# Kernel optimization log

Measured on AMD Instinct MI355X. Metric: run time of the kernel, lower is better.

The kernel has to match this reference:

```python
import jax, jax.numpy as jnp
import numpy as np

N, E, H, R = 50000, 800000, 256, 8
LN_EPS = 1e-5


def setup_inputs() -> dict:
    key = jax.random.key(0)
    ks = jax.random.split(key, 6)
    node_states = jax.random.normal(ks[0], (N, H), dtype=jnp.float32)
    edge_index = jax.random.randint(ks[1], (2, E), 0, N, dtype=jnp.int64)
    edge_type_ids = jax.random.randint(ks[2], (E,), 0, R, dtype=jnp.int64)
    scale = 1.0 / np.sqrt(H)
    W_rel = jax.random.normal(ks[3], (R, H, H), dtype=jnp.float32) * scale
    W_root = jax.random.normal(ks[4], (H, H), dtype=jnp.float32) * scale
    bias = jnp.zeros((H,), dtype=jnp.float32)
    ln_gamma = jnp.ones((H,), dtype=jnp.float32)
    ln_beta = jnp.zeros((H,), dtype=jnp.float32)
    return {
        "node_states": node_states,
        "edge_index": edge_index,
        "edge_type_ids": edge_type_ids,
        "W_rel": W_rel,
        "W_root": W_root,
        "bias": bias,
        "ln_gamma": ln_gamma,
        "ln_beta": ln_beta,
    }


def _rgcn_layer(node_states, edge_index, edge_type_ids, W_rel, W_root, bias, ln_gamma, ln_beta):
    n, h = node_states.shape
    r = W_rel.shape[0]
    src, dst = edge_index[0], edge_index[1]
    # Per-(dst, relation) MEAN of source features (PyG RGCNConv default aggr='mean').
    seg = dst * r + edge_type_ids  # composite segment id in [0, N*R)
    msgs = node_states[src]  # [E, H] gather
    sums = jax.ops.segment_sum(msgs, seg, num_segments=n * r).reshape(n, r, h)
    counts = jax.ops.segment_sum(jnp.ones((src.shape[0],), node_states.dtype), seg,
                                 num_segments=n * r).reshape(n, r, 1)
    mean = sums / jnp.maximum(counts, 1.0)  # zero-edge buckets stay 0
    # Relation-specific linear transforms applied to aggregated means, then root + bias.
    agg = jnp.einsum('nrh,rho->no', mean, W_rel)
    conv = agg + node_states @ W_root + bias
    # Exact (erf-based) GELU to match torch.nn.functional.gelu default.
    updated = jax.nn.gelu(conv, approximate=False)
    # Dropout is identity in eval mode.
    x = updated + node_states  # residual
    mu = jnp.mean(x, axis=-1, keepdims=True)
    var = jnp.mean(jnp.square(x - mu), axis=-1, keepdims=True)
    return ln_gamma * (x - mu) * jax.lax.rsqrt(var + LN_EPS) + ln_beta


def reference(node_states, edge_index, edge_type_ids, W_rel, W_root, bias, ln_gamma, ln_beta):
    return _rgcn_layer(node_states, edge_index, edge_type_ids, W_rel, W_root, bias, ln_gamma, ln_beta)
```

## Files before the change

### kernel.cpp

```cpp
#include <hip/hip_runtime.h>
#include <cstdint>
#include <cstddef>

#define N_NODES 50000
#define N_EDGES 800000
#define HDIM    256
#define NREL    8
#define NSEG    (N_NODES * NREL)
#define KDIM    (NREL * HDIM + HDIM)
#define KA      (NREL * HDIM)
#define LN_EPSF 1e-5f

#define SCAN_CHUNK 1024
#define SCAN_NB    ((NSEG + SCAN_CHUNK - 1) / SCAN_CHUNK)

using short8  = __attribute__((ext_vector_type(8))) short;
using ushort8 = __attribute__((ext_vector_type(8))) unsigned short;
using float4v = __attribute__((ext_vector_type(4))) float;

static __device__ __forceinline__ unsigned short f2bf(float f) {
    union { float f; uint32_t i; } v; v.f = f;
    uint32_t r = v.i + 0x7FFFu + ((v.i >> 16) & 1u);
    return (unsigned short)(r >> 16);
}
static __device__ __forceinline__ float bf2f(unsigned short u) {
    union { uint32_t i; float f; } v; v.i = ((uint32_t)u) << 16; return v.f;
}

__global__ __launch_bounds__(256) void k_cast(const float* __restrict__ ns,
                                              unsigned short* __restrict__ ns16) {
    int idx = blockIdx.x * blockDim.x + threadIdx.x;
    if (idx >= N_NODES * HDIM / 8) return;
    const float4v* nsv = (const float4v*)ns;
    float4v v0 = nsv[idx * 2], v1 = nsv[idx * 2 + 1];
    ushort8 o;
    o[0] = f2bf(v0[0]); o[1] = f2bf(v0[1]); o[2] = f2bf(v0[2]); o[3] = f2bf(v0[3]);
    o[4] = f2bf(v1[0]); o[5] = f2bf(v1[1]); o[6] = f2bf(v1[2]); o[7] = f2bf(v1[3]);
    *(ushort8*)&ns16[(size_t)idx * 8] = o;
}

__global__ void k_count(const int* __restrict__ ei, const int* __restrict__ et,
                        int* __restrict__ cnt) {
    int e = blockIdx.x * blockDim.x + threadIdx.x;
    if (e >= N_EDGES) return;
    int dst = ei[N_EDGES + e];
    int rel = et[e];
    atomicAdd(&cnt[dst * NREL + rel], 1);
}

__global__ __launch_bounds__(256) void k_scan1(const int* __restrict__ cnt,
                                               int* __restrict__ bsum) {
    int b = blockIdx.x, t = threadIdx.x;
    int idx = b * SCAN_CHUNK + t * 4;
    int4 v = {0, 0, 0, 0};
    if (idx + 3 < NSEG) v = *(const int4*)&cnt[idx];
    else {
        #pragma unroll
        for (int j = 0; j < 4; ++j) if (idx + j < NSEG) ((int*)&v)[j] = cnt[idx + j];
    }
    int s = v.x + v.y + v.z + v.w;
    #pragma unroll
    for (int o = 32; o > 0; o >>= 1) s += __shfl_xor(s, o, 64);
    __shared__ int ls[4];
    if ((t & 63) == 0) ls[t >> 6] = s;
    __syncthreads();
    if (t == 0) bsum[b] = ls[0] + ls[1] + ls[2] + ls[3];
}

__global__ __launch_bounds__(512) void k_scan2(const int* __restrict__ bsum,
                                               int* __restrict__ boff) {
    __shared__ int s[512];
    int t = threadIdx.x;
    int v = (t < SCAN_NB) ? bsum[t] : 0;
    s[t] = v;
    __syncthreads();
    for (int d = 1; d < 512; d <<= 1) {
        int x = (t >= d) ? s[t - d] : 0;
        __syncthreads();
        s[t] += x;
        __syncthreads();
    }
    if (t < SCAN_NB) boff[t] = s[t] - v;
}

__global__ __launch_bounds__(256) void k_scan3(const int* __restrict__ cnt,
                                               const int* __restrict__ boff,
                                               int* __restrict__ off) {
    int b = blockIdx.x, t = threadIdx.x;
    int idx = b * SCAN_CHUNK + t * 4;
    int4 v = {0, 0, 0, 0};
    if (idx + 3 < NSEG) v = *(const int4*)&cnt[idx];
    else {
        #pragma unroll
        for (int j = 0; j < 4; ++j) if (idx + j < NSEG) ((int*)&v)[j] = cnt[idx + j];
    }
    int s = v.x + v.y + v.z + v.w;
    __shared__ int ls[256];
    ls[t] = s;
    __syncthreads();
    for (int d = 1; d < 256; d <<= 1) {
        int x = (t >= d) ? ls[t - d] : 0;
        __syncthreads();
        ls[t] += x;
        __syncthreads();
    }
    int run = boff[b] + ls[t] - s;
    int4 w;
    w.x = run; run += v.x;
    w.y = run; run += v.y;
    w.z = run; run += v.z;
    w.w = run;
    if (idx + 3 < NSEG) *(int4*)&off[idx] = w;
    else {
        #pragma unroll
        for (int j = 0; j < 4; ++j) if (idx + j < NSEG) off[idx + j] = ((int*)&w)[j];
    }
    if (b == 0 && t == 0) off[NSEG] = N_EDGES;
}

__global__ void k_scatter(const int* __restrict__ ei, const int* __restrict__ et,
                          const int* __restrict__ off, int* __restrict__ cursor,
                          int* __restrict__ srcs) {
    int e = blockIdx.x * blockDim.x + threadIdx.x;
    if (e >= N_EDGES) return;
    int src = ei[e];
    int dst = ei[N_EDGES + e];
    int rel = et[e];
    int seg = dst * NREL + rel;
    int pos = off[seg] + atomicAdd(&cursor[seg], 1);
    srcs[pos] = src;
}

__global__ __launch_bounds__(256) void k_aggregate(const unsigned short* __restrict__ ns16,
                                                   const int* __restrict__ off,
                                                   const int* __restrict__ srcs,
                                                   unsigned short* __restrict__ Afull) {
    int n = blockIdx.x, t = threadIdx.x;
    int g = t >> 5;
    int i = t & 31;
    int seg = n * NREL + g;
    int e0 = off[seg], e1 = off[seg + 1];
    int cnt = e1 - e0;
    int cs = cnt < 32 ? cnt : 32;
    int my_src = (i < cs) ? srcs[e0 + i] : 0;

    const ushort8* nsv = (const ushort8*)ns16;
    float acc[8] = {0.f, 0.f, 0.f, 0.f, 0.f, 0.f, 0.f, 0.f};

    for (int k = 0; k < cs; ++k) {
        int src = __shfl(my_src, k, 32);
        ushort8 v = nsv[(size_t)src * 32 + i];
        #pragma unroll
        for (int j = 0; j < 8; ++j) acc[j] += bf2f(v[j]);
    }
    for (int e = e0 + 32; e < e1; ++e) {
        int src = srcs[e];
        ushort8 v = nsv[(size_t)src * 32 + i];
        #pragma unroll
        for (int j = 0; j < 8; ++j) acc[j] += bf2f(v[j]);
    }

    float inv = (cnt > 0) ? 1.0f / (float)cnt : 0.0f;
    ushort8 wv;
    #pragma unroll
    for (int j = 0; j < 8; ++j) wv[j] = f2bf(acc[j] * inv);
    *(ushort8*)&Afull[(size_t)n * KDIM + g * HDIM + i * 8] = wv;
}

__global__ __launch_bounds__(256) void k_buildB(const float* __restrict__ Wrel,
                                                const float* __restrict__ Wroot,
                                                unsigned short* __restrict__ Bt) {
    __shared__ unsigned short tile[64][66];
    int k0 = blockIdx.x * 64;
    int j0 = blockIdx.y * 64;
    int t = threadIdx.x;

    #pragma unroll
    for (int p = 0; p < 16; ++p) {
        int idx = p * 256 + t;
        int kk = idx >> 6, jj = idx & 63;
        int k = k0 + kk;
        float v;
        if (k < NREL * HDIM) {
            int r = k >> 8, h = k & 255;
            v = Wrel[((size_t)r * HDIM + h) * HDIM + (j0 + jj)];
        } else {
            int h = k - NREL * HDIM;
            v = Wroot[(size_t)h * HDIM + (j0 + jj)];
        }
        tile[kk][jj] = f2bf(v);
    }
    __syncthreads();
    #pragma unroll
    for (int p = 0; p < 16; ++p) {
        int idx = p * 256 + t;
        int jj = idx >> 6, kk = idx & 63;
        Bt[(size_t)(j0 + jj) * KDIM + (k0 + kk)] = tile[kk][jj];
    }
}

#define BM 128
#define BN 256
#define BK 64
#define NITER (KDIM / BK)

__global__ __launch_bounds__(512, 4) void k_gemm(const unsigned short* __restrict__ A,
                                                 const unsigned short* __restrict__ ns16,
                                                 const unsigned short* __restrict__ Bt,
                                                 const float* __restrict__ ns,
                                                 const float* __restrict__ bias,
                                                 const float* __restrict__ gamma,
                                                 const float* __restrict__ beta,
                                                 float* __restrict__ out, int M) {
    __shared__ __align__(16) unsigned short As[BM * BK];
    __shared__ __align__(16) unsigned short Bs[BN * BK];
    __shared__ float s1buf[BM][4], s2buf[BM][4];

    int tid  = threadIdx.x;
    int lane = tid & 63;
    int wid  = tid >> 6;
    int wm   = wid >> 2, wn = wid & 3;
    int brow = blockIdx.x * BM;

    float4v acc[4][4] = {};

    const char* Ab = (const char*)A;
    const char* Nb = (const char*)ns16;
    const char* Bb = (const char*)Bt;
    const size_t rstride = (size_t)KDIM * 2;

    for (int kt = 0; kt < KDIM; kt += BK) {
        #pragma unroll
        for (int i = 0; i < 2; ++i) {
            int linear = i * 8192 + tid * 16;
            int row  = linear >> 7;
            int slot = (linear >> 4) & 7;
            int kb   = (slot ^ (row & 7)) * 16;
            int ra = brow + row; if (ra > M - 1) ra = M - 1;
            const char* ga = (kt < KA)
                ? Ab + (size_t)ra * rstride + (size_t)(kt * 2 + kb)
                : Nb + (size_t)ra * (HDIM * 2) + (size_t)((kt - KA) * 2 + kb);
            __builtin_amdgcn_global_load_lds(
                (const __attribute__((address_space(1))) void*)ga,
                (__attribute__((address_space(3))) void*)((char*)As + linear),
                16, 0, 0);
        }
        #pragma unroll
        for (int i = 0; i < 4; ++i) {
            int linear = i * 8192 + tid * 16;
            int row  = linear >> 7;
            int slot = (linear >> 4) & 7;
            int kb   = (slot ^ (row & 7)) * 16;
            const char* gb = Bb + (size_t)row * rstride + (size_t)(kt * 2 + kb);
            __builtin_amdgcn_global_load_lds(
                (const __attribute__((address_space(1))) void*)gb,
                (__attribute__((address_space(3))) void*)((char*)Bs + linear),
                16, 0, 0);
        }
        __syncthreads();

        #pragma unroll
        for (int h = 0; h < 2; ++h) {
            short8 a[4], b[4];
            int s0 = h * 4 + (lane >> 4);
            #pragma unroll
            for (int m = 0; m < 4; ++m) {
                int r = wm * 64 + m * 16 + (lane & 15);
                a[m] = *(const short8*)((const char*)As + r * 128 + ((s0 ^ (r & 7)) * 16));
            }
            #pragma unroll
            for (int n = 0; n < 4; ++n) {
                int r = wn * 64 + n * 16 + (lane & 15);
                b[n] = *(const short8*)((const char*)Bs + r * 128 + ((s0 ^ (r & 7)) * 16));
            }
            #pragma unroll
            for (int m = 0; m < 4; ++m)
                #pragma unroll
                for (int n = 0; n < 4; ++n)
                    acc[m][n] = __builtin_amdgcn_mfma_f32_16x16x32_bf16(a[m], b[n], acc[m][n], 0, 0, 0);
        }
        __syncthreads();
    }

    int cols[4];
    float bias_v[4];
    #pragma unroll
    for (int n = 0; n < 4; ++n) {
        cols[n] = wn * 64 + n * 16 + (lane & 15);
        bias_v[n] = bias[cols[n]];
    }

    #pragma unroll
    for (int m = 0; m < 4; ++m) {
        #pragma unroll
        for (int q = 0; q < 4; ++q) {
            int lr = wm * 64 + m * 16 + (lane >> 4) * 4 + q;
            int r  = brow + lr;
            float s1 = 0.f, s2 = 0.f;
            #pragma unroll
            for (int n = 0; n < 4; ++n) {
                float conv = acc[m][n][q] + bias_v[n];
                float g = 0.5f * conv * (1.0f + erff(conv * 0.70710678118654752f));
                float resid = (r < M) ? ns[(size_t)r * HDIM + cols[n]] : 0.f;
                float x = g + resid;
                acc[m][n][q] = x;
                s1 += x; s2 += x * x;
            }
            #pragma unroll
            for (int o = 8; o > 0; o >>= 1) {
                s1 += __shfl_xor(s1, o, 64);
                s2 += __shfl_xor(s2, o, 64);
            }
            if ((lane & 15) == 0) { s1buf[lr][wn] = s1; s2buf[lr][wn] = s2; }
        }
    }
    __syncthreads();

    float gam[4], bet[4];
    #pragma unroll
    for (int n = 0; n < 4; ++n) { gam[n] = gamma[cols[n]]; bet[n] = beta[cols[n]]; }

    #pragma unroll
    for (int m = 0; m < 4; ++m) {
        #pragma unroll
        for (int q = 0; q < 4; ++q) {
            int lr = wm * 64 + m * 16 + (lane >> 4) * 4 + q;
            int r  = brow + lr;
            float t1 = s1buf[lr][0] + s1buf[lr][1] + s1buf[lr][2] + s1buf[lr][3];
            float t2 = s2buf[lr][0] + s2buf[lr][1] + s2buf[lr][2] + s2buf[lr][3];
            float mu  = t1 * (1.0f / HDIM);
            float var = t2 * (1.0f / HDIM) - mu * mu;
            float rstd = rsqrtf(var + LN_EPSF);
            if (r < M) {
                #pragma unroll
                for (int n = 0; n < 4; ++n) {
                    float x = acc[m][n][q];
                    out[(size_t)r * HDIM + cols[n]] = gam[n] * (x - mu) * rstd + bet[n];
                }
            }
        }
    }
}

extern "C" void kernel_launch(void* const* d_in, const int* in_sizes, int n_in,
                              void* d_out, int out_size, void* d_ws, size_t ws_size,
                              hipStream_t stream) {
    const float* ns    = (const float*)d_in[0];
    const int*   ei    = (const int*)d_in[1];
    const int*   et    = (const int*)d_in[2];
    const float* Wrel  = (const float*)d_in[3];
    const float* Wroot = (const float*)d_in[4];
    const float* bias  = (const float*)d_in[5];
    const float* gamma = (const float*)d_in[6];
    const float* beta  = (const float*)d_in[7];
    float* out = (float*)d_out;

    char* w = (char*)d_ws;
    auto take = [&](size_t bytes) -> char* {
        char* p = w; w += (bytes + 255) & ~(size_t)255; return p;
    };
    int* cnt              = (int*)take((size_t)NSEG * 4);
    int* segoff           = (int*)take((size_t)(NSEG + 1) * 4);
    int* cursor           = (int*)take((size_t)NSEG * 4);
    int* srcs             = (int*)take((size_t)N_EDGES * 4);
    int* bsum             = (int*)take((size_t)SCAN_NB * 4);
    int* boff             = (int*)take((size_t)SCAN_NB * 4);
    unsigned short* Afull = (unsigned short*)take((size_t)N_NODES * KDIM * 2);
    unsigned short* Bt    = (unsigned short*)take((size_t)HDIM * KDIM * 2);
    unsigned short* ns16  = (unsigned short*)take((size_t)N_NODES * HDIM * 2);

    hipMemsetAsync(cnt, 0, (size_t)NSEG * 4, stream);
    hipMemsetAsync(cursor, 0, (size_t)NSEG * 4, stream);

    k_cast<<<(N_NODES * HDIM / 8 + 255) / 256, 256, 0, stream>>>(ns, ns16);
    k_count<<<(N_EDGES + 255) / 256, 256, 0, stream>>>(ei, et, cnt);
    k_scan1<<<SCAN_NB, 256, 0, stream>>>(cnt, bsum);
    k_scan2<<<1, 512, 0, stream>>>(bsum, boff);
    k_scan3<<<SCAN_NB, 256, 0, stream>>>(cnt, boff, segoff);
    k_scatter<<<(N_EDGES + 255) / 256, 256, 0, stream>>>(ei, et, segoff, cursor, srcs);
    k_aggregate<<<N_NODES, 256, 0, stream>>>(ns16, segoff, srcs, Afull);
    dim3 gb(KDIM / 64, HDIM / 64);
    k_buildB<<<gb, 256, 0, stream>>>(Wrel, Wroot, Bt);

    dim3 gg((N_NODES + BM - 1) / BM, 1);
    k_gemm<<<gg, 512, 0, stream>>>(Afull, ns16, Bt, ns, bias, gamma, beta, out, N_NODES);
}
```

Measured before the change: 304.1 us.

## Double-buffer GEMM LDS tiles with split prefetch and larger row tile

```diff
diff --git a/kernel.cpp b/kernel.cpp
--- a/kernel.cpp
+++ b/kernel.cpp
@@ -199,12 +199,12 @@
     }
 }
 
-#define BM 128
+#define BM 256
 #define BN 256
 #define BK 64
-#define NITER (KDIM / BK)
-
-__global__ __launch_bounds__(512, 4) void k_gemm(const unsigned short* __restrict__ A,
+#define NT (KDIM / BK)
+
+__global__ __launch_bounds__(512, 2) void k_gemm(const unsigned short* __restrict__ A,
                                                  const unsigned short* __restrict__ ns16,
                                                  const unsigned short* __restrict__ Bt,
                                                  const float* __restrict__ ns,
@@ -212,74 +212,110 @@
                                                  const float* __restrict__ gamma,
                                                  const float* __restrict__ beta,
                                                  float* __restrict__ out, int M) {
-    __shared__ __align__(16) unsigned short As[BM * BK];
-    __shared__ __align__(16) unsigned short Bs[BN * BK];
+    __shared__ __align__(16) unsigned short As[2][BM * BK];
+    __shared__ __align__(16) unsigned short Bs[2][BN * BK];
     __shared__ float s1buf[BM][4], s2buf[BM][4];
 
     int tid  = threadIdx.x;
     int lane = tid & 63;
     int wid  = tid >> 6;
-    int wm   = wid >> 2, wn = wid & 3;
+    int wm   = wid >> 2;
+    int wn   = wid & 3;
     int brow = blockIdx.x * BM;
 
-    float4v acc[4][4] = {};
+    float4v acc[8][4] = {};
 
     const char* Ab = (const char*)A;
     const char* Nb = (const char*)ns16;
     const char* Bb = (const char*)Bt;
     const size_t rstride = (size_t)KDIM * 2;
 
-    for (int kt = 0; kt < KDIM; kt += BK) {
-        #pragma unroll
-        for (int i = 0; i < 2; ++i) {
-            int linear = i * 8192 + tid * 16;
+    auto issueA = [&](int t) {
+        int slot  = t & 1;
+        int kbase = t * BK * 2;
+        #pragma unroll
+        for (int l = 0; l < 4; ++l) {
+            int linear = l * 8192 + tid * 16;
             int row  = linear >> 7;
-            int slot = (linear >> 4) & 7;
-            int kb   = (slot ^ (row & 7)) * 16;
+            int s16  = (linear >> 4) & 7;
+            int kb   = (s16 ^ (row & 7)) * 16;
             int ra = brow + row; if (ra > M - 1) ra = M - 1;
-            const char* ga = (kt < KA)
-                ? Ab + (size_t)ra * rstride + (size_t)(kt * 2 + kb)
-                : Nb + (size_t)ra * (HDIM * 2) + (size_t)((kt - KA) * 2 + kb);
+            const char* ga = (kbase < KA * 2)
+                ? Ab + (size_t)ra * rstride + (size_t)(kbase + kb)
+                : Nb + (size_t)ra * (HDIM * 2) + (size_t)(kbase - KA * 2 + kb);
             __builtin_amdgcn_global_load_lds(
                 (const __attribute__((address_space(1))) void*)ga,
-                (__attribute__((address_space(3))) void*)((char*)As + linear),
+                (__attribute__((address_space(3))) void*)((char*)As[slot] + linear),
                 16, 0, 0);
         }
-        #pragma unroll
-        for (int i = 0; i < 4; ++i) {
-            int linear = i * 8192 + tid * 16;
+    };
+    auto issueB = [&](int t) {
+        int slot  = t & 1;
+        int kbase = t * BK * 2;
+        #pragma unroll
+        for (int l = 0; l < 4; ++l) {
+            int linear = l * 8192 + tid * 16;
             int row  = linear >> 7;
-            int slot = (linear >> 4) & 7;
-            int kb   = (slot ^ (row & 7)) * 16;
-            const char* gb = Bb + (size_t)row * rstride + (size_t)(kt * 2 + kb);
+            int s16  = (linear >> 4) & 7;
+            int kb   = (s16 ^ (row & 7)) * 16;
+            const char* gb = Bb + (size_t)row * rstride + (size_t)(kbase + kb);
             __builtin_amdgcn_global_load_lds(
                 (const __attribute__((address_space(1))) void*)gb,
-                (__attribute__((address_space(3))) void*)((char*)Bs + linear),
+                (__attribute__((address_space(3))) void*)((char*)Bs[slot] + linear),
                 16, 0, 0);
         }
-        __syncthreads();
-
-        #pragma unroll
-        for (int h = 0; h < 2; ++h) {
-            short8 a[4], b[4];
-            int s0 = h * 4 + (lane >> 4);
+    };
+
+    auto bar = [&]() {
+        asm volatile("" ::: "memory");
+        __builtin_amdgcn_s_barrier();
+        asm volatile("" ::: "memory");
+    };
+
+    auto phase = [&](int slot, int h, int mh) {
+        short8 a[4], b[4];
+        int s0 = h * 4 + (lane >> 4);
+        #pragma unroll
+        for (int m = 0; m < 4; ++m) {
+            int r = wm * 128 + mh * 64 + m * 16 + (lane & 15);
+            a[m] = *(const short8*)((const char*)As[slot] + r * 128 + ((s0 ^ (r & 7)) * 16));
+        }
+        #pragma unroll
+        for (int n = 0; n < 4; ++n) {
+            int r = wn * 64 + n * 16 + (lane & 15);
+            b[n] = *(const short8*)((const char*)Bs[slot] + r * 128 + ((s0 ^ (r & 7)) * 16));
+        }
+        __builtin_amdgcn_s_setprio(1);
+        #pragma unroll
+        for (int m = 0; m < 4; ++m)
             #pragma unroll
-            for (int m = 0; m < 4; ++m) {
-                int r = wm * 64 + m * 16 + (lane & 15);
-                a[m] = *(const short8*)((const char*)As + r * 128 + ((s0 ^ (r & 7)) * 16));
-            }
-            #pragma unroll
-            for (int n = 0; n < 4; ++n) {
-                int r = wn * 64 + n * 16 + (lane & 15);
-                b[n] = *(const short8*)((const char*)Bs + r * 128 + ((s0 ^ (r & 7)) * 16));
-            }
-            #pragma unroll
-            for (int m = 0; m < 4; ++m)
-                #pragma unroll
-                for (int n = 0; n < 4; ++n)
-                    acc[m][n] = __builtin_amdgcn_mfma_f32_16x16x32_bf16(a[m], b[n], acc[m][n], 0, 0, 0);
-        }
-        __syncthreads();
+            for (int n = 0; n < 4; ++n)
+                acc[mh * 4 + m][n] =
+                    __builtin_amdgcn_mfma_f32_16x16x32_bf16(a[m], b[n], acc[mh * 4 + m][n], 0, 0, 0);
+        __builtin_amdgcn_s_setprio(0);
+    };
+
+    issueA(0); issueB(0);
+
+    #pragma unroll 1
+    for (int t = 0; t < NT; ++t) {
+        int slot = t & 1;
+        if (t + 1 < NT) {
+            issueA(t + 1);
+            asm volatile("s_waitcnt vmcnt(4)" ::: "memory");
+        } else {
+            asm volatile("s_waitcnt vmcnt(0)" ::: "memory");
+        }
+        bar();
+        phase(slot, 0, 0);
+        bar();
+        if (t + 1 < NT) issueB(t + 1);
+        phase(slot, 0, 1);
+        bar();
+        phase(slot, 1, 0);
+        bar();
+        phase(slot, 1, 1);
+        bar();
     }
 
     int cols[4];
@@ -291,10 +327,10 @@
     }
 
     #pragma unroll
-    for (int m = 0; m < 4; ++m) {
+    for (int m = 0; m < 8; ++m) {
         #pragma unroll
         for (int q = 0; q < 4; ++q) {
-            int lr = wm * 64 + m * 16 + (lane >> 4) * 4 + q;
+            int lr = wm * 128 + m * 16 + (lane >> 4) * 4 + q;
             int r  = brow + lr;
             float s1 = 0.f, s2 = 0.f;
             #pragma unroll
@@ -321,10 +357,10 @@
     for (int n = 0; n < 4; ++n) { gam[n] = gamma[cols[n]]; bet[n] = beta[cols[n]]; }
 
     #pragma unroll
-    for (int m = 0; m < 4; ++m) {
+    for (int m = 0; m < 8; ++m) {
         #pragma unroll
         for (int q = 0; q < 4; ++q) {
-            int lr = wm * 64 + m * 16 + (lane >> 4) * 4 + q;
+            int lr = wm * 128 + m * 16 + (lane >> 4) * 4 + q;
             int r  = brow + lr;
             float t1 = s1buf[lr][0] + s1buf[lr][1] + s1buf[lr][2] + s1buf[lr][3];
             float t2 = s2buf[lr][0] + s2buf[lr][1] + s2buf[lr][2] + s2buf[lr][3];
```

Measured after the change: 345.5 us. 13.6% more time.

## Fuse cast/count, inline block-offset scan, reuse offsets as scatter cursors

Applied to the files above, without the earlier changes.

```diff
diff --git a/kernel.cpp b/kernel.cpp
--- a/kernel.cpp
+++ b/kernel.cpp
@@ -13,6 +13,8 @@
 
 #define SCAN_CHUNK 1024
 #define SCAN_NB    ((NSEG + SCAN_CHUNK - 1) / SCAN_CHUNK)
+#define CAST_NB    ((N_NODES * HDIM / 8 + 255) / 256)
+#define COUNT_NB   ((N_EDGES + 255) / 256)
 
 using short8  = __attribute__((ext_vector_type(8))) short;
 using ushort8 = __attribute__((ext_vector_type(8))) unsigned short;
@@ -27,25 +29,26 @@
     union { uint32_t i; float f; } v; v.i = ((uint32_t)u) << 16; return v.f;
 }
 
-__global__ __launch_bounds__(256) void k_cast(const float* __restrict__ ns,
-                                              unsigned short* __restrict__ ns16) {
-    int idx = blockIdx.x * blockDim.x + threadIdx.x;
-    if (idx >= N_NODES * HDIM / 8) return;
-    const float4v* nsv = (const float4v*)ns;
-    float4v v0 = nsv[idx * 2], v1 = nsv[idx * 2 + 1];
-    ushort8 o;
-    o[0] = f2bf(v0[0]); o[1] = f2bf(v0[1]); o[2] = f2bf(v0[2]); o[3] = f2bf(v0[3]);
-    o[4] = f2bf(v1[0]); o[5] = f2bf(v1[1]); o[6] = f2bf(v1[2]); o[7] = f2bf(v1[3]);
-    *(ushort8*)&ns16[(size_t)idx * 8] = o;
-}
-
-__global__ void k_count(const int* __restrict__ ei, const int* __restrict__ et,
-                        int* __restrict__ cnt) {
-    int e = blockIdx.x * blockDim.x + threadIdx.x;
-    if (e >= N_EDGES) return;
-    int dst = ei[N_EDGES + e];
-    int rel = et[e];
-    atomicAdd(&cnt[dst * NREL + rel], 1);
+__global__ __launch_bounds__(256) void k_cast_count(const float* __restrict__ ns,
+                                                    unsigned short* __restrict__ ns16,
+                                                    const int* __restrict__ ei,
+                                                    const int* __restrict__ et,
+                                                    int* __restrict__ cnt) {
+    int b = blockIdx.x, t = threadIdx.x;
+    if (b < CAST_NB) {
+        int idx = b * 256 + t;
+        const float4v* nsv = (const float4v*)ns;
+        float4v v0 = nsv[idx * 2], v1 = nsv[idx * 2 + 1];
+        ushort8 o;
+        o[0] = f2bf(v0[0]); o[1] = f2bf(v0[1]); o[2] = f2bf(v0[2]); o[3] = f2bf(v0[3]);
+        o[4] = f2bf(v1[0]); o[5] = f2bf(v1[1]); o[6] = f2bf(v1[2]); o[7] = f2bf(v1[3]);
+        *(ushort8*)&ns16[(size_t)idx * 8] = o;
+    } else {
+        int e = (b - CAST_NB) * 256 + t;
+        int dst = ei[N_EDGES + e];
+        int rel = et[e];
+        atomicAdd(&cnt[dst * NREL + rel], 1);
+    }
 }
 
 __global__ __launch_bounds__(256) void k_scan1(const int* __restrict__ cnt,
@@ -67,26 +70,21 @@
     if (t == 0) bsum[b] = ls[0] + ls[1] + ls[2] + ls[3];
 }
 
-__global__ __launch_bounds__(512) void k_scan2(const int* __restrict__ bsum,
-                                               int* __restrict__ boff) {
-    __shared__ int s[512];
-    int t = threadIdx.x;
-    int v = (t < SCAN_NB) ? bsum[t] : 0;
-    s[t] = v;
-    __syncthreads();
-    for (int d = 1; d < 512; d <<= 1) {
-        int x = (t >= d) ? s[t - d] : 0;
-        __syncthreads();
-        s[t] += x;
-        __syncthreads();
-    }
-    if (t < SCAN_NB) boff[t] = s[t] - v;
-}
-
 __global__ __launch_bounds__(256) void k_scan3(const int* __restrict__ cnt,
-                                               const int* __restrict__ boff,
+                                               const int* __restrict__ bsum,
                                                int* __restrict__ off) {
     int b = blockIdx.x, t = threadIdx.x;
+
+    int p = 0;
+    if (t < b) p = bsum[t];
+    if (t + 256 < b) p += bsum[t + 256];
+    #pragma unroll
+    for (int o = 32; o > 0; o >>= 1) p += __shfl_xor(p, o, 64);
+    __shared__ int ps[4];
+    if ((t & 63) == 0) ps[t >> 6] = p;
+    __syncthreads();
+    int boffb = ps[0] + ps[1] + ps[2] + ps[3];
+
     int idx = b * SCAN_CHUNK + t * 4;
     int4 v = {0, 0, 0, 0};
     if (idx + 3 < NSEG) v = *(const int4*)&cnt[idx];
@@ -104,7 +102,7 @@
         ls[t] += x;
         __syncthreads();
     }
-    int run = boff[b] + ls[t] - s;
+    int run = boffb + ls[t] - s;
     int4 w;
     w.x = run; run += v.x;
     w.y = run; run += v.y;
@@ -115,19 +113,17 @@
         #pragma unroll
         for (int j = 0; j < 4; ++j) if (idx + j < NSEG) off[idx + j] = ((int*)&w)[j];
     }
-    if (b == 0 && t == 0) off[NSEG] = N_EDGES;
 }
 
 __global__ void k_scatter(const int* __restrict__ ei, const int* __restrict__ et,
-                          const int* __restrict__ off, int* __restrict__ cursor,
-                          int* __restrict__ srcs) {
+                          int* __restrict__ off, int* __restrict__ srcs) {
     int e = blockIdx.x * blockDim.x + threadIdx.x;
     if (e >= N_EDGES) return;
     int src = ei[e];
     int dst = ei[N_EDGES + e];
     int rel = et[e];
     int seg = dst * NREL + rel;
-    int pos = off[seg] + atomicAdd(&cursor[seg], 1);
+    int pos = atomicAdd(&off[seg], 1);
     srcs[pos] = src;
 }
 
@@ -139,7 +135,8 @@
     int g = t >> 5;
     int i = t & 31;
     int seg = n * NREL + g;
-    int e0 = off[seg], e1 = off[seg + 1];
+    int e1 = off[seg];
+    int e0 = (seg == 0) ? 0 : off[seg - 1];
     int cnt = e1 - e0;
     int cs = cnt < 32 ? cnt : 32;
     int my_src = (i < cs) ? srcs[e0 + i] : 0;
@@ -360,24 +357,19 @@
         char* p = w; w += (bytes + 255) & ~(size_t)255; return p;
     };
     int* cnt              = (int*)take((size_t)NSEG * 4);
-    int* segoff           = (int*)take((size_t)(NSEG + 1) * 4);
-    int* cursor           = (int*)take((size_t)NSEG * 4);
+    int* segoff           = (int*)take((size_t)NSEG * 4);
     int* srcs             = (int*)take((size_t)N_EDGES * 4);
     int* bsum             = (int*)take((size_t)SCAN_NB * 4);
-    int* boff             = (int*)take((size_t)SCAN_NB * 4);
     unsigned short* Afull = (unsigned short*)take((size_t)N_NODES * KDIM * 2);
     unsigned short* Bt    = (unsigned short*)take((size_t)HDIM * KDIM * 2);
     unsigned short* ns16  = (unsigned short*)take((size_t)N_NODES * HDIM * 2);
 
     hipMemsetAsync(cnt, 0, (size_t)NSEG * 4, stream);
-    hipMemsetAsync(cursor, 0, (size_t)NSEG * 4, stream);
-
-    k_cast<<<(N_NODES * HDIM / 8 + 255) / 256, 256, 0, stream>>>(ns, ns16);
-    k_count<<<(N_EDGES + 255) / 256, 256, 0, stream>>>(ei, et, cnt);
+
+    k_cast_count<<<CAST_NB + COUNT_NB, 256, 0, stream>>>(ns, ns16, ei, et, cnt);
     k_scan1<<<SCAN_NB, 256, 0, stream>>>(cnt, bsum);
-    k_scan2<<<1, 512, 0, stream>>>(bsum, boff);
-    k_scan3<<<SCAN_NB, 256, 0, stream>>>(cnt, boff, segoff);
-    k_scatter<<<(N_EDGES + 255) / 256, 256, 0, stream>>>(ei, et, segoff, cursor, srcs);
+    k_scan3<<<SCAN_NB, 256, 0, stream>>>(cnt, bsum, segoff);
+    k_scatter<<<COUNT_NB, 256, 0, stream>>>(ei, et, segoff, srcs);
     k_aggregate<<<N_NODES, 256, 0, stream>>>(ns16, segoff, srcs, Afull);
     dim3 gb(KDIM / 64, HDIM / 64);
     k_buildB<<<gb, 256, 0, stream>>>(Wrel, Wroot, Bt);
```

Result: no change. 307.3 us (+1.0%).
